# Optimization experiments

Hardware: AMD Instinct MI355X
Metric: run time of the kernel (lower is better)

Reference implementation:

```python
import jax, jax.numpy as jnp
import numpy as np

E = 1024  # input_dimension
D = 64    # output_dimension (head dim)

def setup_inputs() -> dict:
    key = jax.random.key(0)
    k1, k2, k3, k4 = jax.random.split(key, 4)
    x = jax.random.normal(k1, (4, 4096, E), dtype=jnp.float32)
    # Linear(E, D, bias=False): y = x @ W.T with W of shape [D, E]; store as [E, D]
    Wq = jax.random.normal(k2, (E, D), dtype=jnp.float32) / np.sqrt(E)
    Wk = jax.random.normal(k3, (E, D), dtype=jnp.float32) / np.sqrt(E)
    Wv = jax.random.normal(k4, (E, D), dtype=jnp.float32) / np.sqrt(E)
    return {"x": x, "Wq": Wq, "Wk": Wk, "Wv": Wv}

def reference(x, Wq, Wk, Wv):
    # q,k,v: [B, T, D]
    q = jnp.einsum('bte,ed->btd', x, Wq)
    k = jnp.einsum('bte,ed->btd', x, Wk)
    v = jnp.einsum('bte,ed->btd', x, Wv)
    # NOTE: faithful to source: softmax is UNscaled; 1/sqrt(D) applied AFTER A@V
    scores = jnp.einsum('bqd,bkd->bqk', q, k)          # [B, T, T]
    weights = jax.nn.softmax(scores, axis=-1)
    out = jnp.einsum('bqk,bkd->bqd', weights, v) / jnp.sqrt(jnp.float32(D))
    return out
```

## Files before the change

kernel.cpp:

```cpp
#include <hip/hip_runtime.h>
#include <hip/hip_bf16.h>
#include <stdint.h>

#define B_ 4
#define T_ 4096
#define E_ 1024
#define D_ 64
#define NSPLIT 8
#define KCHUNK (T_ / NSPLIT)

typedef short s16x8 __attribute__((ext_vector_type(8)));
typedef float f32x4 __attribute__((ext_vector_type(4)));

static __device__ __forceinline__ unsigned short f2bf(float f) {
    unsigned int u = __builtin_bit_cast(unsigned int, f);
    u += 0x7fffu + ((u >> 16) & 1u);
    return (unsigned short)(u >> 16);
}
static __device__ __forceinline__ float bf2f(unsigned short s) {
    unsigned int u = ((unsigned int)s) << 16;
    return __builtin_bit_cast(float, u);
}


__global__ __launch_bounds__(256) void wsplit_kernel(
    const float* __restrict__ Wq, const float* __restrict__ Wk,
    const float* __restrict__ Wv,
    unsigned short* __restrict__ wfh, unsigned short* __restrict__ wfl)
{
    int f = blockIdx.x * 256 + threadIdx.x;
    int m = f >> 16;
    int rem = f & 65535;
    int e = rem >> 6, d = rem & 63;
    const float* W = (m == 0) ? Wq : (m == 1) ? Wk : Wv;
    float v = W[(size_t)e * D_ + d];
    unsigned short hi = f2bf(v);
    int col = m * 64 + d;
    size_t o = ((size_t)((col >> 4) * 32 + (e >> 5)) * 64
                + ((col & 15) + 16 * ((e & 31) >> 3))) * 8 + (e & 7);
    wfh[o] = hi;
    wfl[o] = f2bf(v - bf2f(hi));
}

__global__ __launch_bounds__(256) void proj_kernel(
    const float* __restrict__ x,
    const unsigned short* __restrict__ wfh, const unsigned short* __restrict__ wfl,
    unsigned short* __restrict__ qfh, unsigned short* __restrict__ qfl,
    unsigned short* __restrict__ kfh, unsigned short* __restrict__ kfl,
    unsigned short* __restrict__ vf)
{
    __shared__ unsigned short xh[32 * 72];
    __shared__ unsigned short xl[32 * 72];
    const int tid = threadIdx.x;
    const int ln  = tid & 63;
    const int wv  = tid >> 6;
    const int lq  = ln & 15;
    const int lg  = ln >> 4;
    const int row0 = blockIdx.x * 32;

    f32x4 acc[2][3];
#pragma unroll
    for (int rf = 0; rf < 2; ++rf)
#pragma unroll
        for (int ct = 0; ct < 3; ++ct) acc[rf][ct] = (f32x4){0.f, 0.f, 0.f, 0.f};

    const unsigned short* pwh0 = wfh + ((size_t)((wv * 3 + 0) * 32) * 64 + ln) * 8;
    const unsigned short* pwh1 = wfh + ((size_t)((wv * 3 + 1) * 32) * 64 + ln) * 8;
    const unsigned short* pwh2 = wfh + ((size_t)((wv * 3 + 2) * 32) * 64 + ln) * 8;
    const unsigned short* pwl0 = wfl + ((size_t)((wv * 3 + 0) * 32) * 64 + ln) * 8;
    const unsigned short* pwl1 = wfl + ((size_t)((wv * 3 + 1) * 32) * 64 + ln) * 8;
    const unsigned short* pwl2 = wfl + ((size_t)((wv * 3 + 2) * 32) * 64 + ln) * 8;

    float2 xv[4];
#pragma unroll
    for (int jj = 0; jj < 4; ++jj) {
        int idx = tid + jj * 256;
        int r = idx >> 5, c2 = (idx & 31) * 2;
        xv[jj] = *(const float2*)(x + (size_t)(row0 + r) * E_ + c2);
    }

    for (int kcs = 0; kcs < 16; ++kcs) {
#pragma unroll
        for (int jj = 0; jj < 4; ++jj) {
            int idx = tid + jj * 256;
            int r = idx >> 5, c2 = (idx & 31) * 2;
            unsigned short h0 = f2bf(xv[jj].x), h1 = f2bf(xv[jj].y);
            *(ushort2*)&xh[r * 72 + c2] = (ushort2){h0, h1};
            *(ushort2*)&xl[r * 72 + c2] = (ushort2){f2bf(xv[jj].x - bf2f(h0)),
                                                    f2bf(xv[jj].y - bf2f(h1))};
        }
        __syncthreads();
        if (kcs < 15) {
            int kc = (kcs + 1) * 64;
#pragma unroll
            for (int jj = 0; jj < 4; ++jj) {
                int idx = tid + jj * 256;
                int r = idx >> 5, c2 = (idx & 31) * 2;
                xv[jj] = *(const float2*)(x + (size_t)(row0 + r) * E_ + kc + c2);
            }
        }

        s16x8 ah[2][2], al[2][2];
#pragma unroll
        for (int rf = 0; rf < 2; ++rf)
#pragma unroll
            for (int hh = 0; hh < 2; ++hh) {
                ah[rf][hh] = *(const s16x8*)&xh[(rf * 16 + lq) * 72 + hh * 32 + lg * 8];
                al[rf][hh] = *(const s16x8*)&xl[(rf * 16 + lq) * 72 + hh * 32 + lg * 8];
            }
#pragma unroll
        for (int hh = 0; hh < 2; ++hh) {
            s16x8 bh0 = *(const s16x8*)(pwh0 + hh * 512);
            s16x8 bl0 = *(const s16x8*)(pwl0 + hh * 512);
            s16x8 bh1 = *(const s16x8*)(pwh1 + hh * 512);
            s16x8 bl1 = *(const s16x8*)(pwl1 + hh * 512);
            s16x8 bh2 = *(const s16x8*)(pwh2 + hh * 512);
            s16x8 bl2 = *(const s16x8*)(pwl2 + hh * 512);
#pragma unroll
            for (int rf = 0; rf < 2; ++rf) {
                acc[rf][0] = __builtin_amdgcn_mfma_f32_16x16x32_bf16(ah[rf][hh], bh0, acc[rf][0], 0, 0, 0);
                acc[rf][0] = __builtin_amdgcn_mfma_f32_16x16x32_bf16(al[rf][hh], bh0, acc[rf][0], 0, 0, 0);
                acc[rf][0] = __builtin_amdgcn_mfma_f32_16x16x32_bf16(ah[rf][hh], bl0, acc[rf][0], 0, 0, 0);
                acc[rf][1] = __builtin_amdgcn_mfma_f32_16x16x32_bf16(ah[rf][hh], bh1, acc[rf][1], 0, 0, 0);
                acc[rf][1] = __builtin_amdgcn_mfma_f32_16x16x32_bf16(al[rf][hh], bh1, acc[rf][1], 0, 0, 0);
                acc[rf][1] = __builtin_amdgcn_mfma_f32_16x16x32_bf16(ah[rf][hh], bl1, acc[rf][1], 0, 0, 0);
                acc[rf][2] = __builtin_amdgcn_mfma_f32_16x16x32_bf16(ah[rf][hh], bh2, acc[rf][2], 0, 0, 0);
                acc[rf][2] = __builtin_amdgcn_mfma_f32_16x16x32_bf16(al[rf][hh], bh2, acc[rf][2], 0, 0, 0);
                acc[rf][2] = __builtin_amdgcn_mfma_f32_16x16x32_bf16(ah[rf][hh], bl2, acc[rf][2], 0, 0, 0);
            }
        }
        pwh0 += 1024; pwh1 += 1024; pwh2 += 1024;
        pwl0 += 1024; pwl1 += 1024; pwl2 += 1024;
        __syncthreads();
    }

#pragma unroll
    for (int rf = 0; rf < 2; ++rf)
#pragma unroll
        for (int ct = 0; ct < 3; ++ct) {
            int col = wv * 48 + ct * 16 + lq;
            int m = col >> 6;
            int d = col & 63;
#pragma unroll
            for (int j = 0; j < 4; ++j) {
                int row = row0 + rf * 16 + 4 * lg + j;
                float val = acc[rf][ct][j];
                if (m == 0) {
                    unsigned short hi = f2bf(val);
                    size_t o = ((size_t)((row >> 4) * 2 + (d >> 5)) * 64
                                + ((row & 15) + 16 * ((d & 31) >> 3))) * 8 + (d & 7);
                    qfh[o] = hi;
                    qfl[o] = f2bf(val - bf2f(hi));
                } else if (m == 1) {
                    unsigned short hi = f2bf(val);
                    size_t o = ((size_t)((row >> 4) * 2 + (d >> 5)) * 64
                                + ((row & 15) + 16 * ((d & 31) >> 3))) * 8 + (d & 7);
                    kfh[o] = hi;
                    kfl[o] = f2bf(val - bf2f(hi));
                } else {
                    int b = row >> 12, t = row & 4095;
                    int p = ((t & 15) << 1) | ((t >> 4) & 1);
                    size_t o = ((size_t)((b * 128 + (t >> 5)) * 4 + (d >> 4)) * 64
                                + ((d & 15) + 16 * (p >> 3))) * 8 + (p & 7);
                    vf[o] = f2bf(val);
                }
            }
        }
}

__global__ __launch_bounds__(256) void attn_kernel(
    const unsigned short* __restrict__ qfh, const unsigned short* __restrict__ qfl,
    const unsigned short* __restrict__ kfh, const unsigned short* __restrict__ kfl,
    const unsigned short* __restrict__ vf,
    float* __restrict__ po, float* __restrict__ pl)
{
    __shared__ __align__(16) unsigned int p_lds[4][16][20];
    const int tid = threadIdx.x;
    const int ln  = tid & 63;
    const int wvq = tid >> 6;

    int bid = blockIdx.x;
    int swz = (bid & 7) * 256 + (bid >> 3);
    int wid = swz * 4 + wvq;
    const int split = wid >> 10;
    const int tile  = wid & 1023;
    const int b     = tile >> 8;
    const int trow  = (tile & 255) * 16;
    const int kv0   = split * KCHUNK;

    const int lq = ln & 15;
    const int lg = ln >> 4;
    const int qb = lg * 4;

    const int t16q = (b * T_ + trow) >> 4;
    s16x8 qhf[2], qlf[2];
#pragma unroll
    for (int h = 0; h < 2; ++h) {
        size_t off = (size_t)t16q * 1024 + h * 512 + ln * 8;
        qhf[h] = *(const s16x8*)(qfh + off);
        qlf[h] = *(const s16x8*)(qfl + off);
    }

    const int t16k0 = (b * T_ + kv0) >> 4;
    const unsigned short* pkh = kfh + (size_t)t16k0 * 1024 + ln * 8;
    const unsigned short* pkl = kfl + (size_t)t16k0 * 1024 + ln * 8;
    const unsigned short* pvv = vf + (size_t)(b * 128 + (kv0 >> 5)) * 2048 + ln * 8;

    f32x4 o[4];
#pragma unroll
    for (int dt = 0; dt < 4; ++dt) o[dt] = (f32x4){0.f, 0.f, 0.f, 0.f};
    float lsum[4] = {0.f, 0.f, 0.f, 0.f};

    const float LOG2E = 1.44269504f;
    const float CEXP  = 20.0f * 1.44269504f;

    for (int it = 0; it < KCHUNK / 32; ++it) {
        f32x4 s0 = {0.f, 0.f, 0.f, 0.f}, s1 = {0.f, 0.f, 0.f, 0.f};
        {
            s16x8 kh00 = *(const s16x8*)(pkh);
            s16x8 kl00 = *(const s16x8*)(pkl);
            s16x8 kh01 = *(const s16x8*)(pkh + 512);
            s16x8 kl01 = *(const s16x8*)(pkl + 512);
            s0 = __builtin_amdgcn_mfma_f32_16x16x32_bf16(qhf[0], kh00, s0, 0, 0, 0);
            s0 = __builtin_amdgcn_mfma_f32_16x16x32_bf16(qlf[0], kh00, s0, 0, 0, 0);
            s0 = __builtin_amdgcn_mfma_f32_16x16x32_bf16(qhf[0], kl00, s0, 0, 0, 0);
            s0 = __builtin_amdgcn_mfma_f32_16x16x32_bf16(qhf[1], kh01, s0, 0, 0, 0);
            s0 = __builtin_amdgcn_mfma_f32_16x16x32_bf16(qlf[1], kh01, s0, 0, 0, 0);
            s0 = __builtin_amdgcn_mfma_f32_16x16x32_bf16(qhf[1], kl01, s0, 0, 0, 0);
            s16x8 kh10 = *(const s16x8*)(pkh + 1024);
            s16x8 kl10 = *(const s16x8*)(pkl + 1024);
            s16x8 kh11 = *(const s16x8*)(pkh + 1536);
            s16x8 kl11 = *(const s16x8*)(pkl + 1536);
            s1 = __builtin_amdgcn_mfma_f32_16x16x32_bf16(qhf[0], kh10, s1, 0, 0, 0);
            s1 = __builtin_amdgcn_mfma_f32_16x16x32_bf16(qlf[0], kh10, s1, 0, 0, 0);
            s1 = __builtin_amdgcn_mfma_f32_16x16x32_bf16(qhf[0], kl10, s1, 0, 0, 0);
            s1 = __builtin_amdgcn_mfma_f32_16x16x32_bf16(qhf[1], kh11, s1, 0, 0, 0);
            s1 = __builtin_amdgcn_mfma_f32_16x16x32_bf16(qlf[1], kh11, s1, 0, 0, 0);
            s1 = __builtin_amdgcn_mfma_f32_16x16x32_bf16(qhf[1], kl11, s1, 0, 0, 0);
        }
#pragma unroll
        for (int j = 0; j < 4; ++j) {
            float p0 = __builtin_exp2f(__builtin_fmaf(s0[j], LOG2E, -CEXP));
            float p1 = __builtin_exp2f(__builtin_fmaf(s1[j], LOG2E, -CEXP));
            lsum[j] += p0 + p1;
            unsigned int pk = ((unsigned int)f2bf(p1) << 16) | (unsigned int)f2bf(p0);
            p_lds[wvq][qb + j][lq] = pk;
        }
        s16x8 pa = *(const s16x8*)&p_lds[wvq][lq][4 * lg];

#pragma unroll
        for (int dt = 0; dt < 4; ++dt) {
            s16x8 vfr = *(const s16x8*)(pvv + dt * 512);
            o[dt] = __builtin_amdgcn_mfma_f32_16x16x32_bf16(pa, vfr, o[dt], 0, 0, 0);
        }
        pkh += 2048; pkl += 2048; pvv += 2048;
    }

#pragma unroll
    for (int j = 0; j < 4; ++j)
#pragma unroll
        for (int dt = 0; dt < 4; ++dt)
            po[(size_t)wid * 1024 + (qb + j) * 64 + dt * 16 + lq] = o[dt][j];

#pragma unroll
    for (int off = 1; off < 16; off <<= 1) {
#pragma unroll
        for (int j = 0; j < 4; ++j) lsum[j] += __shfl_xor(lsum[j], off);
    }
    if (lq == 0) {
#pragma unroll
        for (int j = 0; j < 4; ++j)
            pl[(size_t)wid * 16 + qb + j] = lsum[j];
    }
}

__global__ __launch_bounds__(256) void attn_combine_kernel(
    const float* __restrict__ po, const float* __restrict__ pl,
    float* __restrict__ out)
{
    const int qt = blockIdx.x;
    const int tid = threadIdx.x;
    const int d  = tid & 63;
    const int rg = tid >> 6;
    const int b = qt >> 8;
    const int trow = (qt & 255) * 16;

#pragma unroll
    for (int ri = 0; ri < 4; ++ri) {
        int row = rg * 4 + ri;
        float den = 0.f, acc = 0.f;
#pragma unroll
        for (int s = 0; s < NSPLIT; ++s) {
            den += pl[((size_t)(s * 1024 + qt)) * 16 + row];
            acc += po[((size_t)(s * 1024 + qt)) * 1024 + row * 64 + d];
        }
        out[((size_t)(b * T_) + trow + row) * D_ + d] = acc / (den * 8.0f);
    }
}

extern "C" void kernel_launch(void* const* d_in, const int* in_sizes, int n_in,
                              void* d_out, int out_size, void* d_ws, size_t ws_size,
                              hipStream_t stream)
{
    const float* x  = (const float*)d_in[0];
    const float* Wq = (const float*)d_in[1];
    const float* Wk = (const float*)d_in[2];
    const float* Wv = (const float*)d_in[3];
    float* out = (float*)d_out;

    char* w = (char*)d_ws;
    float* po = (float*)w;                       w += (size_t)8192 * 1024 * 4;
    float* pl = (float*)w;                       w += (size_t)8192 * 16 * 4;
    unsigned short* qfh = (unsigned short*)w;    w += (size_t)B_ * T_ * D_ * 2;
    unsigned short* qfl = (unsigned short*)w;    w += (size_t)B_ * T_ * D_ * 2;
    unsigned short* kfh = (unsigned short*)w;    w += (size_t)B_ * T_ * D_ * 2;
    unsigned short* kfl = (unsigned short*)w;    w += (size_t)B_ * T_ * D_ * 2;
    unsigned short* vf  = (unsigned short*)w;    w += (size_t)B_ * T_ * D_ * 2;
    unsigned short* wfh = (unsigned short*)w;    w += (size_t)192 * E_ * 2;
    unsigned short* wfl = (unsigned short*)w;    w += (size_t)192 * E_ * 2;

    hipLaunchKernelGGL(wsplit_kernel, dim3(768), dim3(256), 0, stream,
                       Wq, Wk, Wv, wfh, wfl);
    hipLaunchKernelGGL(proj_kernel, dim3(512), dim3(256), 0, stream,
                       x, wfh, wfl, qfh, qfl, kfh, kfl, vf);
    hipLaunchKernelGGL(attn_kernel, dim3(2048), dim3(256), 0, stream,
                       qfh, qfl, kfh, kfl, vf, po, pl);
    hipLaunchKernelGGL(attn_combine_kernel, dim3(1024), dim3(256), 0, stream,
                       po, pl, out);
}
```

Measured before the change: 186.4 us.

## Double-buffer K fragments in attention and shrink projection tiles to 16 rows

The attention loop now prefetches the next K hi/lo fragments into a second register set while computing the current step. Score accumulation is split into two independent MFMA chains to shorten dependency latency. The projection kernel uses 16-row tiles with twice as many blocks, float4 loads, packed bf16 conversion via v_cvt_pk_bf16_f32, and split accumulators. These changes raise register pressure and give up reuse of W fragments across two row tiles.

```diff
diff --git a/kernel.cpp b/kernel.cpp
--- a/kernel.cpp
+++ b/kernel.cpp
@@ -20,6 +20,14 @@
 static __device__ __forceinline__ float bf2f(unsigned short s) {
     unsigned int u = ((unsigned int)s) << 16;
     return __builtin_bit_cast(float, u);
+}
+static __device__ __forceinline__ float asf(unsigned int u) {
+    return __builtin_bit_cast(float, u);
+}
+static __device__ __forceinline__ unsigned int cvtpk(float a, float b) {
+    unsigned int r;
+    asm("v_cvt_pk_bf16_f32 %0, %1, %2" : "=v"(r) : "v"(a), "v"(b));
+    return r;
 }
 
 
@@ -49,123 +57,158 @@
     unsigned short* __restrict__ kfh, unsigned short* __restrict__ kfl,
     unsigned short* __restrict__ vf)
 {
-    __shared__ unsigned short xh[32 * 72];
-    __shared__ unsigned short xl[32 * 72];
+    __shared__ unsigned short xh[16 * 72];
+    __shared__ unsigned short xl[16 * 72];
     const int tid = threadIdx.x;
     const int ln  = tid & 63;
     const int wv  = tid >> 6;
     const int lq  = ln & 15;
     const int lg  = ln >> 4;
-    const int row0 = blockIdx.x * 32;
-
-    f32x4 acc[2][3];
-#pragma unroll
-    for (int rf = 0; rf < 2; ++rf)
-#pragma unroll
-        for (int ct = 0; ct < 3; ++ct) acc[rf][ct] = (f32x4){0.f, 0.f, 0.f, 0.f};
-
-    const unsigned short* pwh0 = wfh + ((size_t)((wv * 3 + 0) * 32) * 64 + ln) * 8;
-    const unsigned short* pwh1 = wfh + ((size_t)((wv * 3 + 1) * 32) * 64 + ln) * 8;
-    const unsigned short* pwh2 = wfh + ((size_t)((wv * 3 + 2) * 32) * 64 + ln) * 8;
-    const unsigned short* pwl0 = wfl + ((size_t)((wv * 3 + 0) * 32) * 64 + ln) * 8;
-    const unsigned short* pwl1 = wfl + ((size_t)((wv * 3 + 1) * 32) * 64 + ln) * 8;
-    const unsigned short* pwl2 = wfl + ((size_t)((wv * 3 + 2) * 32) * 64 + ln) * 8;
-
-    float2 xv[4];
-#pragma unroll
-    for (int jj = 0; jj < 4; ++jj) {
-        int idx = tid + jj * 256;
-        int r = idx >> 5, c2 = (idx & 31) * 2;
-        xv[jj] = *(const float2*)(x + (size_t)(row0 + r) * E_ + c2);
-    }
+    const int row0 = blockIdx.x * 16;
+
+    f32x4 accA[3], accB[3];
+#pragma unroll
+    for (int ct = 0; ct < 3; ++ct) {
+        accA[ct] = (f32x4){0.f, 0.f, 0.f, 0.f};
+        accB[ct] = (f32x4){0.f, 0.f, 0.f, 0.f};
+    }
+
+    const unsigned short* pwh[3];
+    const unsigned short* pwl[3];
+#pragma unroll
+    for (int ct = 0; ct < 3; ++ct) {
+        pwh[ct] = wfh + ((size_t)((wv * 3 + ct) * 32) * 64 + ln) * 8;
+        pwl[ct] = wfl + ((size_t)((wv * 3 + ct) * 32) * 64 + ln) * 8;
+    }
+
+    const int sr = tid >> 4;
+    const int sc = (tid & 15) * 4;
+    const float* xrow = x + (size_t)(row0 + sr) * E_ + sc;
+    float4 xv = *(const float4*)(xrow);
 
     for (int kcs = 0; kcs < 16; ++kcs) {
-#pragma unroll
-        for (int jj = 0; jj < 4; ++jj) {
-            int idx = tid + jj * 256;
-            int r = idx >> 5, c2 = (idx & 31) * 2;
-            unsigned short h0 = f2bf(xv[jj].x), h1 = f2bf(xv[jj].y);
-            *(ushort2*)&xh[r * 72 + c2] = (ushort2){h0, h1};
-            *(ushort2*)&xl[r * 72 + c2] = (ushort2){f2bf(xv[jj].x - bf2f(h0)),
-                                                    f2bf(xv[jj].y - bf2f(h1))};
+        unsigned int h01 = cvtpk(xv.x, xv.y);
+        unsigned int h23 = cvtpk(xv.z, xv.w);
+        float rx = xv.x - asf(h01 << 16);
+        float ry = xv.y - asf(h01 & 0xffff0000u);
+        float rz = xv.z - asf(h23 << 16);
+        float rw = xv.w - asf(h23 & 0xffff0000u);
+        unsigned int l01 = cvtpk(rx, ry);
+        unsigned int l23 = cvtpk(rz, rw);
+        *(uint2*)&xh[sr * 72 + sc] = (uint2){h01, h23};
+        *(uint2*)&xl[sr * 72 + sc] = (uint2){l01, l23};
+        __syncthreads();
+        if (kcs < 15) xv = *(const float4*)(xrow + (kcs + 1) * 64);
+
+        s16x8 ah0 = *(const s16x8*)&xh[lq * 72 + lg * 8];
+        s16x8 ah1 = *(const s16x8*)&xh[lq * 72 + 32 + lg * 8];
+        s16x8 al0 = *(const s16x8*)&xl[lq * 72 + lg * 8];
+        s16x8 al1 = *(const s16x8*)&xl[lq * 72 + 32 + lg * 8];
+#pragma unroll
+        for (int ct = 0; ct < 3; ++ct) {
+            s16x8 bh0 = *(const s16x8*)(pwh[ct]);
+            s16x8 bh1 = *(const s16x8*)(pwh[ct] + 512);
+            s16x8 bl0 = *(const s16x8*)(pwl[ct]);
+            s16x8 bl1 = *(const s16x8*)(pwl[ct] + 512);
+            accA[ct] = __builtin_amdgcn_mfma_f32_16x16x32_bf16(ah0, bh0, accA[ct], 0, 0, 0);
+            accA[ct] = __builtin_amdgcn_mfma_f32_16x16x32_bf16(ah1, bh1, accA[ct], 0, 0, 0);
+            accA[ct] = __builtin_amdgcn_mfma_f32_16x16x32_bf16(ah0, bl0, accA[ct], 0, 0, 0);
+            accB[ct] = __builtin_amdgcn_mfma_f32_16x16x32_bf16(al0, bh0, accB[ct], 0, 0, 0);
+            accB[ct] = __builtin_amdgcn_mfma_f32_16x16x32_bf16(al1, bh1, accB[ct], 0, 0, 0);
+            accB[ct] = __builtin_amdgcn_mfma_f32_16x16x32_bf16(ah1, bl1, accB[ct], 0, 0, 0);
+            pwh[ct] += 1024;
+            pwl[ct] += 1024;
         }
         __syncthreads();
-        if (kcs < 15) {
-            int kc = (kcs + 1) * 64;
-#pragma unroll
-            for (int jj = 0; jj < 4; ++jj) {
-                int idx = tid + jj * 256;
-                int r = idx >> 5, c2 = (idx & 31) * 2;
-                xv[jj] = *(const float2*)(x + (size_t)(row0 + r) * E_ + kc + c2);
+    }
+
+#pragma unroll
+    for (int ct = 0; ct < 3; ++ct) {
+        int col = wv * 48 + ct * 16 + lq;
+        int m = col >> 6;
+        int d = col & 63;
+#pragma unroll
+        for (int j = 0; j < 4; ++j) {
+            int row = row0 + 4 * lg + j;
+            float val = accA[ct][j] + accB[ct][j];
+            if (m == 0) {
+                unsigned short hi = f2bf(val);
+                size_t o = ((size_t)((row >> 4) * 2 + (d >> 5)) * 64
+                            + ((row & 15) + 16 * ((d & 31) >> 3))) * 8 + (d & 7);
+                qfh[o] = hi;
+                qfl[o] = f2bf(val - bf2f(hi));
+            } else if (m == 1) {
+                unsigned short hi = f2bf(val);
+                size_t o = ((size_t)((row >> 4) * 2 + (d >> 5)) * 64
+                            + ((row & 15) + 16 * ((d & 31) >> 3))) * 8 + (d & 7);
+                kfh[o] = hi;
+                kfl[o] = f2bf(val - bf2f(hi));
+            } else {
+                int b = row >> 12, t = row & 4095;
+                int p = ((t & 15) << 1) | ((t >> 4) & 1);
+                size_t o = ((size_t)((b * 128 + (t >> 5)) * 4 + (d >> 4)) * 64
+                            + ((d & 15) + 16 * (p >> 3))) * 8 + (p & 7);
+                vf[o] = f2bf(val);
             }
         }
-
-        s16x8 ah[2][2], al[2][2];
-#pragma unroll
-        for (int rf = 0; rf < 2; ++rf)
-#pragma unroll
-            for (int hh = 0; hh < 2; ++hh) {
-                ah[rf][hh] = *(const s16x8*)&xh[(rf * 16 + lq) * 72 + hh * 32 + lg * 8];
-                al[rf][hh] = *(const s16x8*)&xl[(rf * 16 + lq) * 72 + hh * 32 + lg * 8];
-            }
-#pragma unroll
-        for (int hh = 0; hh < 2; ++hh) {
-            s16x8 bh0 = *(const s16x8*)(pwh0 + hh * 512);
-            s16x8 bl0 = *(const s16x8*)(pwl0 + hh * 512);
-            s16x8 bh1 = *(const s16x8*)(pwh1 + hh * 512);
-            s16x8 bl1 = *(const s16x8*)(pwl1 + hh * 512);
-            s16x8 bh2 = *(const s16x8*)(pwh2 + hh * 512);
-            s16x8 bl2 = *(const s16x8*)(pwl2 + hh * 512);
-#pragma unroll
-            for (int rf = 0; rf < 2; ++rf) {
-                acc[rf][0] = __builtin_amdgcn_mfma_f32_16x16x32_bf16(ah[rf][hh], bh0, acc[rf][0], 0, 0, 0);
-                acc[rf][0] = __builtin_amdgcn_mfma_f32_16x16x32_bf16(al[rf][hh], bh0, acc[rf][0], 0, 0, 0);
-                acc[rf][0] = __builtin_amdgcn_mfma_f32_16x16x32_bf16(ah[rf][hh], bl0, acc[rf][0], 0, 0, 0);
-                acc[rf][1] = __builtin_amdgcn_mfma_f32_16x16x32_bf16(ah[rf][hh], bh1, acc[rf][1], 0, 0, 0);
-                acc[rf][1] = __builtin_amdgcn_mfma_f32_16x16x32_bf16(al[rf][hh], bh1, acc[rf][1], 0, 0, 0);
-                acc[rf][1] = __builtin_amdgcn_mfma_f32_16x16x32_bf16(ah[rf][hh], bl1, acc[rf][1], 0, 0, 0);
-                acc[rf][2] = __builtin_amdgcn_mfma_f32_16x16x32_bf16(ah[rf][hh], bh2, acc[rf][2], 0, 0, 0);
-                acc[rf][2] = __builtin_amdgcn_mfma_f32_16x16x32_bf16(al[rf][hh], bh2, acc[rf][2], 0, 0, 0);
-                acc[rf][2] = __builtin_amdgcn_mfma_f32_16x16x32_bf16(ah[rf][hh], bl2, acc[rf][2], 0, 0, 0);
-            }
-        }
-        pwh0 += 1024; pwh1 += 1024; pwh2 += 1024;
-        pwl0 += 1024; pwl1 += 1024; pwl2 += 1024;
-        __syncthreads();
-    }
-
-#pragma unroll
-    for (int rf = 0; rf < 2; ++rf)
-#pragma unroll
-        for (int ct = 0; ct < 3; ++ct) {
-            int col = wv * 48 + ct * 16 + lq;
-            int m = col >> 6;
-            int d = col & 63;
-#pragma unroll
-            for (int j = 0; j < 4; ++j) {
-                int row = row0 + rf * 16 + 4 * lg + j;
-                float val = acc[rf][ct][j];
-                if (m == 0) {
-                    unsigned short hi = f2bf(val);
-                    size_t o = ((size_t)((row >> 4) * 2 + (d >> 5)) * 64
-                                + ((row & 15) + 16 * ((d & 31) >> 3))) * 8 + (d & 7);
-                    qfh[o] = hi;
-                    qfl[o] = f2bf(val - bf2f(hi));
-                } else if (m == 1) {
-                    unsigned short hi = f2bf(val);
-                    size_t o = ((size_t)((row >> 4) * 2 + (d >> 5)) * 64
-                                + ((row & 15) + 16 * ((d & 31) >> 3))) * 8 + (d & 7);
-                    kfh[o] = hi;
-                    kfl[o] = f2bf(val - bf2f(hi));
-                } else {
-                    int b = row >> 12, t = row & 4095;
-                    int p = ((t & 15) << 1) | ((t >> 4) & 1);
-                    size_t o = ((size_t)((b * 128 + (t >> 5)) * 4 + (d >> 4)) * 64
-                                + ((d & 15) + 16 * (p >> 3))) * 8 + (p & 7);
-                    vf[o] = f2bf(val);
-                }
-            }
-        }
+    }
+}
+
+struct KF { s16x8 kh[4], kl[4]; };
+
+__device__ __forceinline__ void load_kf(KF& f, const unsigned short* pkh,
+                                        const unsigned short* pkl)
+{
+#pragma unroll
+    for (int i = 0; i < 4; ++i) {
+        f.kh[i] = *(const s16x8*)(pkh + i * 512);
+        f.kl[i] = *(const s16x8*)(pkl + i * 512);
+    }
+}
+
+__device__ __forceinline__ void attn_step(
+    const KF& f, const unsigned short* pvv,
+    const s16x8* qhf, const s16x8* qlf,
+    f32x4* o, float* lsum,
+    unsigned int (*prow)[20],
+    int lq, int lg, int qb)
+{
+    const float LOG2E = 1.44269504f;
+    const float CEXP  = 20.0f * 1.44269504f;
+
+    s16x8 v0 = *(const s16x8*)(pvv);
+    s16x8 v1 = *(const s16x8*)(pvv + 512);
+    s16x8 v2 = *(const s16x8*)(pvv + 1024);
+    s16x8 v3 = *(const s16x8*)(pvv + 1536);
+
+    f32x4 s0a = {0.f,0.f,0.f,0.f}, s0b = {0.f,0.f,0.f,0.f};
+    f32x4 s1a = {0.f,0.f,0.f,0.f}, s1b = {0.f,0.f,0.f,0.f};
+    s0a = __builtin_amdgcn_mfma_f32_16x16x32_bf16(qhf[0], f.kh[0], s0a, 0, 0, 0);
+    s0b = __builtin_amdgcn_mfma_f32_16x16x32_bf16(qlf[0], f.kh[0], s0b, 0, 0, 0);
+    s0a = __builtin_amdgcn_mfma_f32_16x16x32_bf16(qhf[1], f.kh[1], s0a, 0, 0, 0);
+    s0b = __builtin_amdgcn_mfma_f32_16x16x32_bf16(qlf[1], f.kh[1], s0b, 0, 0, 0);
+    s0a = __builtin_amdgcn_mfma_f32_16x16x32_bf16(qhf[0], f.kl[0], s0a, 0, 0, 0);
+    s0b = __builtin_amdgcn_mfma_f32_16x16x32_bf16(qhf[1], f.kl[1], s0b, 0, 0, 0);
+    s1a = __builtin_amdgcn_mfma_f32_16x16x32_bf16(qhf[0], f.kh[2], s1a, 0, 0, 0);
+    s1b = __builtin_amdgcn_mfma_f32_16x16x32_bf16(qlf[0], f.kh[2], s1b, 0, 0, 0);
+    s1a = __builtin_amdgcn_mfma_f32_16x16x32_bf16(qhf[1], f.kh[3], s1a, 0, 0, 0);
+    s1b = __builtin_amdgcn_mfma_f32_16x16x32_bf16(qlf[1], f.kh[3], s1b, 0, 0, 0);
+    s1a = __builtin_amdgcn_mfma_f32_16x16x32_bf16(qhf[0], f.kl[2], s1a, 0, 0, 0);
+    s1b = __builtin_amdgcn_mfma_f32_16x16x32_bf16(qhf[1], f.kl[3], s1b, 0, 0, 0);
+
+#pragma unroll
+    for (int j = 0; j < 4; ++j) {
+        float p0 = __builtin_exp2f(__builtin_fmaf(s0a[j] + s0b[j], LOG2E, -CEXP));
+        float p1 = __builtin_exp2f(__builtin_fmaf(s1a[j] + s1b[j], LOG2E, -CEXP));
+        lsum[j] += p0 + p1;
+        prow[qb + j][lq] = cvtpk(p0, p1);
+    }
+    s16x8 pa = *(const s16x8*)&prow[lq][4 * lg];
+
+    o[0] = __builtin_amdgcn_mfma_f32_16x16x32_bf16(pa, v0, o[0], 0, 0, 0);
+    o[1] = __builtin_amdgcn_mfma_f32_16x16x32_bf16(pa, v1, o[1], 0, 0, 0);
+    o[2] = __builtin_amdgcn_mfma_f32_16x16x32_bf16(pa, v2, o[2], 0, 0, 0);
+    o[3] = __builtin_amdgcn_mfma_f32_16x16x32_bf16(pa, v3, o[3], 0, 0, 0);
 }
 
 __global__ __launch_bounds__(256) void attn_kernel(
@@ -211,49 +254,16 @@
     for (int dt = 0; dt < 4; ++dt) o[dt] = (f32x4){0.f, 0.f, 0.f, 0.f};
     float lsum[4] = {0.f, 0.f, 0.f, 0.f};
 
-    const float LOG2E = 1.44269504f;
-    const float CEXP  = 20.0f * 1.44269504f;
-
-    for (int it = 0; it < KCHUNK / 32; ++it) {
-        f32x4 s0 = {0.f, 0.f, 0.f, 0.f}, s1 = {0.f, 0.f, 0.f, 0.f};
-        {
-            s16x8 kh00 = *(const s16x8*)(pkh);
-            s16x8 kl00 = *(const s16x8*)(pkl);
-            s16x8 kh01 = *(const s16x8*)(pkh + 512);
-            s16x8 kl01 = *(const s16x8*)(pkl + 512);
-            s0 = __builtin_amdgcn_mfma_f32_16x16x32_bf16(qhf[0], kh00, s0, 0, 0, 0);
-            s0 = __builtin_amdgcn_mfma_f32_16x16x32_bf16(qlf[0], kh00, s0, 0, 0, 0);
-            s0 = __builtin_amdgcn_mfma_f32_16x16x32_bf16(qhf[0], kl00, s0, 0, 0, 0);
-            s0 = __builtin_amdgcn_mfma_f32_16x16x32_bf16(qhf[1], kh01, s0, 0, 0, 0);
-            s0 = __builtin_amdgcn_mfma_f32_16x16x32_bf16(qlf[1], kh01, s0, 0, 0, 0);
-            s0 = __builtin_amdgcn_mfma_f32_16x16x32_bf16(qhf[1], kl01, s0, 0, 0, 0);
-            s16x8 kh10 = *(const s16x8*)(pkh + 1024);
-            s16x8 kl10 = *(const s16x8*)(pkl + 1024);
-            s16x8 kh11 = *(const s16x8*)(pkh + 1536);
-            s16x8 kl11 = *(const s16x8*)(pkl + 1536);
-            s1 = __builtin_amdgcn_mfma_f32_16x16x32_bf16(qhf[0], kh10, s1, 0, 0, 0);
-            s1 = __builtin_amdgcn_mfma_f32_16x16x32_bf16(qlf[0], kh10, s1, 0, 0, 0);
-            s1 = __builtin_amdgcn_mfma_f32_16x16x32_bf16(qhf[0], kl10, s1, 0, 0, 0);
-            s1 = __builtin_amdgcn_mfma_f32_16x16x32_bf16(qhf[1], kh11, s1, 0, 0, 0);
-            s1 = __builtin_amdgcn_mfma_f32_16x16x32_bf16(qlf[1], kh11, s1, 0, 0, 0);
-            s1 = __builtin_amdgcn_mfma_f32_16x16x32_bf16(qhf[1], kl11, s1, 0, 0, 0);
-        }
-#pragma unroll
-        for (int j = 0; j < 4; ++j) {
-            float p0 = __builtin_exp2f(__builtin_fmaf(s0[j], LOG2E, -CEXP));
-            float p1 = __builtin_exp2f(__builtin_fmaf(s1[j], LOG2E, -CEXP));
-            lsum[j] += p0 + p1;
-            unsigned int pk = ((unsigned int)f2bf(p1) << 16) | (unsigned int)f2bf(p0);
-            p_lds[wvq][qb + j][lq] = pk;
-        }
-        s16x8 pa = *(const s16x8*)&p_lds[wvq][lq][4 * lg];
-
-#pragma unroll
-        for (int dt = 0; dt < 4; ++dt) {
-            s16x8 vfr = *(const s16x8*)(pvv + dt * 512);
-            o[dt] = __builtin_amdgcn_mfma_f32_16x16x32_bf16(pa, vfr, o[dt], 0, 0, 0);
-        }
-        pkh += 2048; pkl += 2048; pvv += 2048;
+    KF fa, fb;
+    load_kf(fa, pkh, pkl);
+#pragma unroll 1
+    for (int it = 0; it < 8; ++it) {
+        load_kf(fb, pkh + 2048, pkl + 2048);
+        attn_step(fa, pvv, qhf, qlf, o, lsum, p_lds[wvq], lq, lg, qb);
+        pkh += 4096; pkl += 4096;
+        if (it < 7) load_kf(fa, pkh, pkl);
+        attn_step(fb, pvv + 2048, qhf, qlf, o, lsum, p_lds[wvq], lq, lg, qb);
+        pvv += 4096;
     }
 
 #pragma unroll
@@ -321,7 +331,7 @@
 
     hipLaunchKernelGGL(wsplit_kernel, dim3(768), dim3(256), 0, stream,
                        Wq, Wk, Wv, wfh, wfl);
-    hipLaunchKernelGGL(proj_kernel, dim3(512), dim3(256), 0, stream,
+    hipLaunchKernelGGL(proj_kernel, dim3(1024), dim3(256), 0, stream,
                        x, wfh, wfl, qfh, qfl, kfh, kfl, vf);
     hipLaunchKernelGGL(attn_kernel, dim3(2048), dim3(256), 0, stream,
                        qfh, qfl, kfh, kfl, vf, po, pl);
```

After: 198.6 us. 6.5% more time.
